# Performance work log

Hardware: AMD Instinct MI355X
Metric: run time of the kernel (lower is better)

## Reference

```python
import jax, jax.numpy as jnp
import numpy as np

N = 50000      # nodes
E = 800000     # edges
G = 256        # graphs in batch
D_IN = 128     # input_dim
H = 128        # node_hidden_dim
FC = 128       # fc_hidden_dim
OUT = 2        # out_dim
EPS = 1e-5


def _lin_init(key, fan_in, fan_out, bias=True):
    kw, kb = jax.random.split(key)
    w = jax.random.normal(kw, (fan_in, fan_out), jnp.float32) / np.sqrt(fan_in)
    if bias:
        b = jax.random.normal(kb, (fan_out,), jnp.float32) * 0.01
        return w, b
    return w


def setup_inputs() -> dict:
    key = jax.random.key(0)
    ks = jax.random.split(key, 16)
    x = jax.random.normal(ks[0], (N, D_IN), jnp.float32)
    edge_index = jax.random.randint(ks[1], (2, E), 0, N, jnp.int32)
    batch = jnp.sort(jax.random.randint(ks[2], (N,), 0, G, jnp.int32))
    edge_attr = jax.random.uniform(ks[3], (E, 1), jnp.float32)
    # GraphConv params: lin_rel (with bias) + lin_root (no bias)
    w_rel1, b_rel1 = _lin_init(ks[4], D_IN, H)
    w_root1 = _lin_init(ks[5], D_IN, H, bias=False)
    w_rel2, b_rel2 = _lin_init(ks[6], H, 2 * H)
    w_root2 = _lin_init(ks[7], H, 2 * H, bias=False)
    w_rel3, b_rel3 = _lin_init(ks[8], 2 * H, 3 * H)
    w_root3 = _lin_init(ks[9], 2 * H, 3 * H, bias=False)
    # BatchNorm affine params
    gamma1 = jnp.ones((H,), jnp.float32);      beta1 = jnp.zeros((H,), jnp.float32)
    gamma2 = jnp.ones((2 * H,), jnp.float32);  beta2 = jnp.zeros((2 * H,), jnp.float32)
    gamma3 = jnp.ones((3 * H,), jnp.float32);  beta3 = jnp.zeros((3 * H,), jnp.float32)
    # FC head: lin1 in = 3H+6H+9H = 18H
    w_lin1, b_lin1 = _lin_init(ks[10], 18 * H, FC)
    w_lin2, b_lin2 = _lin_init(ks[11], FC, OUT)
    w_lin3, b_lin3 = _lin_init(ks[12], OUT, OUT)
    return dict(x=x, edge_index=edge_index, batch=batch, edge_attr=edge_attr,
                w_rel1=w_rel1, b_rel1=b_rel1, w_root1=w_root1,
                w_rel2=w_rel2, b_rel2=b_rel2, w_root2=w_root2,
                w_rel3=w_rel3, b_rel3=b_rel3, w_root3=w_root3,
                gamma1=gamma1, beta1=beta1, gamma2=gamma2, beta2=beta2,
                gamma3=gamma3, beta3=beta3,
                w_lin1=w_lin1, b_lin1=b_lin1, w_lin2=w_lin2, b_lin2=b_lin2,
                w_lin3=w_lin3, b_lin3=b_lin3)


def _bn(h, gamma, beta):
    # training-mode BatchNorm1d over node axis
    mu = h.mean(0)
    var = h.var(0)
    return (h - mu) * jax.lax.rsqrt(var + EPS) * gamma + beta


def _gconv(h, src, dst, ew, w_rel, b_rel, w_root):
    # PyG GraphConv: lin_rel(sum_j ew_ij * x_j) + lin_root(x_i)
    agg = jax.ops.segment_sum(h[src] * ew[:, None], dst, num_segments=N)
    return agg @ w_rel + b_rel + h @ w_root


def _pool3(h, batch):
    # concat of global max / mean / add pooling per graph
    s = jax.ops.segment_sum(h, batch, num_segments=G)
    cnt = jax.ops.segment_sum(jnp.ones((h.shape[0], 1), h.dtype), batch, num_segments=G)
    mean = s / jnp.maximum(cnt, 1.0)
    m = jax.ops.segment_max(h, batch, num_segments=G)
    m = jnp.where(cnt > 0, m, 0.0)  # guard empty segments
    return jnp.concatenate([m, mean, s], axis=1)


def reference(x, edge_index, batch, edge_attr,
              w_rel1, b_rel1, w_root1, w_rel2, b_rel2, w_root2,
              w_rel3, b_rel3, w_root3,
              gamma1, beta1, gamma2, beta2, gamma3, beta3,
              w_lin1, b_lin1, w_lin2, b_lin2, w_lin3, b_lin3):
    ew = jnp.transpose(edge_attr, (1, 0))[0]            # [E]
    src, dst = edge_index[0], edge_index[1]
    h = _bn(jax.nn.leaky_relu(_gconv(x, src, dst, ew, w_rel1, b_rel1, w_root1)), gamma1, beta1)
    x1 = _pool3(h, batch)
    h = _bn(jax.nn.leaky_relu(_gconv(h, src, dst, ew, w_rel2, b_rel2, w_root2)), gamma2, beta2)
    x2 = _pool3(h, batch)
    h = _bn(jax.nn.leaky_relu(_gconv(h, src, dst, ew, w_rel3, b_rel3, w_root3)), gamma3, beta3)
    x3 = _pool3(h, batch)
    z = jnp.concatenate([x1, x2, x3], axis=1)           # [G, 18H]
    z = jax.nn.relu(z @ w_lin1 + b_lin1)                # dropout is identity in eval
    z = jax.nn.relu(z @ w_lin2 + b_lin2)
    return jax.nn.log_softmax(z @ w_lin3 + b_lin3, axis=-1)
```

## Files before the change

kernel.cpp:

```cpp
#include <hip/hip_runtime.h>
#include <cstdint>
#include <cstddef>

#define N_NODES 50000
#define M_PAD   50048
#define MB_TILES 391
#define N_EDGES 800000
#define N_GRAPH 256
#define Z_DIM   2304
#define NREP    16
#define POOL_TOT (N_GRAPH * (128 + 256 + 384))
#define PP_L1 (MB_TILES * 1 * 2 * 2 * 128)
#define PP_L2 (MB_TILES * 2 * 2 * 2 * 128)
#define PP_L3 (MB_TILES * 3 * 2 * 2 * 128)
#define PP_TOT (PP_L1 + PP_L2 + PP_L3)

static constexpr float LEAKY  = 0.01f;
static constexpr float BN_EPS = 1e-5f;
static constexpr float FNEG   = -3.4e38f;
static constexpr float FPOS   =  3.4e38f;

typedef short short8 __attribute__((ext_vector_type(8)));
typedef float floatx4 __attribute__((ext_vector_type(4)));
typedef const __attribute__((address_space(1))) unsigned int* gas_ptr;
typedef __attribute__((address_space(3))) unsigned int* las_ptr;
typedef unsigned long long ull;

__device__ __forceinline__ unsigned short f2b(float f) {
  union { float f; unsigned int u; } v; v.f = f;
  unsigned int u = v.u;
  unsigned int r = (u + 0x7FFFu + ((u >> 16) & 1u)) >> 16;
  return (unsigned short)r;
}
__device__ __forceinline__ float b2f(unsigned short h) {
  union { unsigned int u; float f; } v; v.u = ((unsigned int)h) << 16;
  return v.f;
}
__device__ __forceinline__ unsigned fkey(float x) {
  unsigned k = __float_as_uint(x);
  return k ^ ((k & 0x80000000u) ? 0xFFFFFFFFu : 0x80000000u);
}
__device__ __forceinline__ float kdec(unsigned k) {
  k ^= (k & 0x80000000u) ? 0x80000000u : 0xFFFFFFFFu;
  return __uint_as_float(k);
}


__global__ void init_all_kernel(int* __restrict__ cntR, int* __restrict__ gcnt,
                                float* __restrict__ sums_all,
                                unsigned* __restrict__ pmaxk, unsigned* __restrict__ pmink,
                                float* __restrict__ psumg) {
  const int i = blockIdx.x * blockDim.x + threadIdx.x;
  if (i < NREP * N_NODES) cntR[i] = 0;
  if (i < N_GRAPH) gcnt[i] = 0;
  if (i < 2 * (128 + 256 + 384)) sums_all[i] = 0.f;
  if (i < POOL_TOT) { pmaxk[i] = 0u; pmink[i] = 0xFFFFFFFFu; psumg[i] = 0.f; }
}


__global__ void hist_rep_kernel(const int* __restrict__ idx, int* __restrict__ cntR, int n) {
  int i = blockIdx.x * blockDim.x + threadIdx.x;
  if (i < n) {
    const int rep = blockIdx.x & (NREP - 1);
    atomicAdd(&cntR[rep * N_NODES + idx[i]], 1);
  }
}

__global__ __launch_bounds__(256) void scan1_fused_kernel(int* __restrict__ cntR,
                                                          int* __restrict__ out,
                                                          int* __restrict__ part, int n) {
  __shared__ int sm[256];
  const int t = threadIdx.x;
  const int base = blockIdx.x * 1024 + t * 4;
  int v[4] = {0, 0, 0, 0};
#pragma unroll
  for (int j = 0; j < 4; ++j) {
    const int d = base + j;
    if (d < n) {
      int s = 0;
#pragma unroll
      for (int r = 0; r < NREP; ++r) {
        const int c = cntR[r * N_NODES + d];
        cntR[r * N_NODES + d] = s;
        s += c;
      }
      v[j] = s;
    }
  }
  const int tsum = v[0] + v[1] + v[2] + v[3];
  sm[t] = tsum;
  __syncthreads();
  for (int off = 1; off < 256; off <<= 1) {
    int x = (t >= off) ? sm[t - off] : 0;
    __syncthreads();
    sm[t] += x;
    __syncthreads();
  }
  const int excl = sm[t] - tsum;
  if (base     < n) out[base]     = excl;
  if (base + 1 < n) out[base + 1] = excl + v[0];
  if (base + 2 < n) out[base + 2] = excl + v[0] + v[1];
  if (base + 3 < n) out[base + 3] = excl + v[0] + v[1] + v[2];
  if (t == 255) part[blockIdx.x] = sm[255];
}

__global__ __launch_bounds__(256) void scan2_kernel(int* __restrict__ part, int nb,
                                                    int* __restrict__ total_out) {
  __shared__ int sm[256];
  const int t = threadIdx.x;
  const int v = (t < nb) ? part[t] : 0;
  sm[t] = v;
  __syncthreads();
  for (int off = 1; off < 256; off <<= 1) {
    int x = (t >= off) ? sm[t - off] : 0;
    __syncthreads();
    sm[t] += x;
    __syncthreads();
  }
  if (t < nb) part[t] = sm[t] - v;
  if (t == 255) *total_out = sm[255];
}

__global__ void scan3_cursor_kernel(int* __restrict__ out, const int* __restrict__ part,
                                    int* __restrict__ cntR, int n) {
  int i = blockIdx.x * blockDim.x + threadIdx.x;
  if (i >= n) return;
  const int rp = out[i] + part[i >> 10];
  out[i] = rp;
#pragma unroll
  for (int r = 0; r < NREP; ++r) cntR[r * N_NODES + i] += rp;
}

__global__ void bucket_kernel(const int* __restrict__ src, const int* __restrict__ dst,
                              const float* __restrict__ ew, int* __restrict__ cntR,
                              ull* __restrict__ epack, int E) {
  int e = blockIdx.x * blockDim.x + threadIdx.x;
  if (e < E) {
    const int rep = blockIdx.x & (NREP - 1);
    const int d = dst[e];
    const int p = atomicAdd(&cntR[rep * N_NODES + d], 1);
    epack[p] = ((ull)__float_as_uint(ew[e]) << 32) | (unsigned)src[e];
  }
}

__global__ __launch_bounds__(256) void hist_batch_kernel(const int* __restrict__ idx,
                                                         int* __restrict__ cnt, int n) {
  __shared__ int lh[N_GRAPH];
  lh[threadIdx.x] = 0;
  __syncthreads();
  int i = blockIdx.x * blockDim.x + threadIdx.x;
  if (i < n) atomicAdd(&lh[idx[i]], 1);
  __syncthreads();
  const int v = lh[threadIdx.x];
  if (v) atomicAdd(&cnt[threadIdx.x], v);
}

__global__ __launch_bounds__(256) void scan256_kernel(const int* __restrict__ cnt,
                                                      int* __restrict__ gptr) {
  __shared__ int sm[256];
  const int t = threadIdx.x;
  const int v = cnt[t];
  sm[t] = v;
  __syncthreads();
  for (int off = 1; off < 256; off <<= 1) {
    int x = (t >= off) ? sm[t - off] : 0;
    __syncthreads();
    sm[t] += x;
    __syncthreads();
  }
  gptr[t] = sm[t] - v;
  if (t == 255) gptr[256] = sm[255];
}


__global__ __launch_bounds__(256) void prep1_kernel(
    const float* __restrict__ x, unsigned short* __restrict__ xb, int npair,
    const float* __restrict__ wrel, const float* __restrict__ wroot,
    const float* __restrict__ brel,
    unsigned short* __restrict__ wt, float* __restrict__ u, float* __restrict__ v) {
  if (blockIdx.x >= 128) {
    const int i = (blockIdx.x - 128) * 256 + threadIdx.x;
    if (i < npair) {
      float2 vv = *(const float2*)(x + 2 * (size_t)i);
      ((unsigned int*)xb)[i] = (unsigned int)f2b(vv.x) | ((unsigned int)f2b(vv.y) << 16);
    }
    return;
  }
  __shared__ float redu[256];
  __shared__ float redv[256];
  const int n = blockIdx.x;
  const int K = 128, N = 128, K2 = 256;
  float us = 0.f, vs = 0.f;
  for (int k = threadIdx.x; k < K2; k += 256) {
    const int kk = (k < K) ? k : k - K;
    const float w = (k < K) ? wrel[(size_t)kk * N + n] : wroot[(size_t)kk * N + n];
    wt[(size_t)n * K2 + k] = f2b(w);
    (void)kk;
  }
  redu[threadIdx.x] = us; redv[threadIdx.x] = vs;
  __syncthreads();
  for (int o = 128; o > 0; o >>= 1) {
    if (threadIdx.x < o) {
      redu[threadIdx.x] += redu[threadIdx.x + o];
      redv[threadIdx.x] += redv[threadIdx.x + o];
    }
    __syncthreads();
  }
  if (threadIdx.x == 0) { u[n] = redu[0]; v[n] = brel[n] + redv[0]; }
}

__global__ __launch_bounds__(256) void wt_build_kernel(
    const float* __restrict__ wrel, const float* __restrict__ wroot,
    const float* __restrict__ brel, const float* __restrict__ sums_prev,
    const float* __restrict__ gamma_prev, const float* __restrict__ beta_prev,
    unsigned short* __restrict__ wt, float* __restrict__ u, float* __restrict__ v,
    int K, int N) {
  __shared__ float redu[256];
  __shared__ float redv[256];
  const int n = blockIdx.x;
  const int K2 = 2 * K;
  const float inv_n = 1.f / (float)N_NODES;
  float us = 0.f, vs = 0.f;
  for (int k = threadIdx.x; k < K2; k += 256) {
    const int kk = (k < K) ? k : k - K;
    const float w = (k < K) ? wrel[(size_t)kk * N + n] : wroot[(size_t)kk * N + n];
    float sc = 1.f, sh = 0.f;
    if (sums_prev) {
      const float mu  = sums_prev[kk] * inv_n;
      const float var = sums_prev[K + kk] * inv_n - mu * mu;
      sc = rsqrtf(var + BN_EPS) * gamma_prev[kk];
      sh = beta_prev[kk] - mu * sc;
    }
    wt[(size_t)n * K2 + k] = f2b(w * sc);
    if (k < K) us += sh * w; else vs += sh * w;
  }
  redu[threadIdx.x] = us; redv[threadIdx.x] = vs;
  __syncthreads();
  for (int o = 128; o > 0; o >>= 1) {
    if (threadIdx.x < o) {
      redu[threadIdx.x] += redu[threadIdx.x + o];
      redv[threadIdx.x] += redv[threadIdx.x + o];
    }
    __syncthreads();
  }
  if (threadIdx.x == 0) { u[n] = redu[0]; v[n] = brel[n] + redv[0]; }
}


template <int D>
__global__ void agg_bf16_kernel(const unsigned short* __restrict__ h,
                                const int* __restrict__ rowptr,
                                const ull* __restrict__ epack,
                                unsigned short* __restrict__ agg,
                                float* __restrict__ degw_out) {
  int gid  = blockIdx.x * blockDim.x + threadIdx.x;
  int node = gid >> 6;
  int lane = threadIdx.x & 63;
  if (node >= N_NODES) return;
  const int beg = rowptr[node], end = rowptr[node + 1];
  constexpr int NP = D / 128;
  float acc0[NP], acc1[NP];
#pragma unroll
  for (int i = 0; i < NP; ++i) { acc0[i] = 0.f; acc1[i] = 0.f; }
  float wsum = 0.f;

  for (int c0 = beg; c0 < end; c0 += 64) {
    const int cn = min(64, end - c0);
    ull pk = 0;
    if (lane < cn) pk = epack[c0 + lane];
    const int   su = (int)(unsigned)pk;
    const float wf = __uint_as_float((unsigned)(pk >> 32));
    const int ng = (cn + 7) >> 3;
    for (int g = 0; g < ng; ++g) {
      int ss[8]; float wv[8];
#pragma unroll
      for (int j = 0; j < 8; ++j) {
        ss[j] = __shfl(su, g * 8 + j);
        wv[j] = __shfl(wf, g * 8 + j);
      }
      unsigned uu[8][NP];
#pragma unroll
      for (int j = 0; j < 8; ++j) {
        const unsigned int* row = (const unsigned int*)(h + (size_t)ss[j] * D);
#pragma unroll
        for (int i = 0; i < NP; ++i) uu[j][i] = row[lane + 64 * i];
      }
#pragma unroll
      for (int j = 0; j < 8; ++j) {
        wsum += wv[j];
#pragma unroll
        for (int i = 0; i < NP; ++i) {
          acc0[i] += b2f((unsigned short)(uu[j][i] & 0xFFFF)) * wv[j];
          acc1[i] += b2f((unsigned short)(uu[j][i] >> 16)) * wv[j];
        }
      }
    }
  }

  unsigned int* o = (unsigned int*)(agg + (size_t)node * D);
#pragma unroll
  for (int i = 0; i < NP; ++i)
    o[lane + 64 * i] = (unsigned int)f2b(acc0[i]) | ((unsigned int)f2b(acc1[i]) << 16);
  if (degw_out != nullptr && lane == 0) degw_out[node] = wsum;
}


__global__ __launch_bounds__(256) void gemm_mfma_kernel(
    const unsigned short* __restrict__ Aagg, const unsigned short* __restrict__ Ah,
    const unsigned short* __restrict__ Wt,
    const float* __restrict__ u, const float* __restrict__ v,
    const float* __restrict__ degw, const int* __restrict__ batch,
    unsigned short* __restrict__ outH, float* __restrict__ sums,
    unsigned* __restrict__ pmaxk, unsigned* __restrict__ pmink,
    float* __restrict__ psumg,
    float* __restrict__ ppmax, float* __restrict__ ppmin, float* __restrict__ ppsum,
    int M, int K, int N) {
  __shared__ char smem[40960];
  unsigned short* AsBase = (unsigned short*)smem;
  unsigned short* BsBase = (unsigned short*)(smem + 24576);
  float* col_s = (float*)smem;
  float* dws   = (float*)(smem + 1024);
  int*   gbs   = (int*)(smem + 1536);

  const int NT = N >> 7;
  const int id = blockIdx.x;
  const int xcd = id & 7;
  const int q   = id >> 3;
  const int m_tile = (q / NT) * 8 + xcd;
  if (m_tile >= MB_TILES) return;
  const int m0 = m_tile * 128;
  const int nt2 = q % NT;
  const int n0 = nt2 * 128;

  const int t  = threadIdx.x;
  const int lane = t & 63;
  const int w    = t >> 6;
  const int wm   = (w & 1) * 64;
  const int wn   = (w >> 1) * 64;
  const int l16  = lane & 15;
  const int lq   = lane >> 4;
  const int K2   = 2 * K;

  const int lrow  = lane >> 2;
  const int lslot = lane & 3;

  floatx4 acc[4][4];
#pragma unroll
  for (int i = 0; i < 4; ++i)
#pragma unroll
    for (int j = 0; j < 4; ++j) acc[i][j] = (floatx4){0.f, 0.f, 0.f, 0.f};

  auto stage_A = [&](unsigned short* Ab, int k0) {
    const unsigned short* Asrc;
    int kbase;
    if (k0 < K) { Asrc = Aagg; kbase = k0; } else { Asrc = Ah; kbase = k0 - K; }
#pragma unroll
    for (int qq = 0; qq < 2; ++qq) {
      const int row = w * 32 + qq * 16 + lrow;
      const int gc  = (lslot ^ ((row >> 1) & 3)) * 8;
      const unsigned short* gA = Asrc + (size_t)(m0 + row) * K + kbase + gc;
      __builtin_amdgcn_global_load_lds((gas_ptr)gA, (las_ptr)(Ab + (w * 32 + qq * 16) * 32),
                                       16, 0, 0);
    }
  };
  auto stage_B = [&](unsigned short* Bb, int k0) {
#pragma unroll
    for (int qq = 0; qq < 2; ++qq) {
      const int row = w * 32 + qq * 16 + lrow;
      const int gc  = (lslot ^ ((row >> 1) & 3)) * 8;
      const unsigned short* gB = Wt + (size_t)(n0 + row) * K2 + k0 + gc;
      __builtin_amdgcn_global_load_lds((gas_ptr)gB, (las_ptr)(Bb + (w * 32 + qq * 16) * 32),
                                       16, 0, 0);
    }
  };

  auto compute = [&](const unsigned short* Ab, const unsigned short* Bb) {
    short8 af[4], bfr[4];
#pragma unroll
    for (int i = 0; i < 4; ++i) {
      const int r = wm + i * 16 + l16;
      af[i] = *(const short8*)(Ab + r * 32 + (lq ^ ((r >> 1) & 3)) * 8);
    }
#pragma unroll
    for (int j = 0; j < 4; ++j) {
      const int r = wn + j * 16 + l16;
      bfr[j] = *(const short8*)(Bb + r * 32 + (lq ^ ((r >> 1) & 3)) * 8);
    }
    __builtin_amdgcn_s_setprio(1);
#pragma unroll
    for (int i = 0; i < 4; ++i)
#pragma unroll
      for (int j = 0; j < 4; ++j)
        acc[i][j] = __builtin_amdgcn_mfma_f32_16x16x32_bf16(af[i], bfr[j], acc[i][j], 0, 0, 0);
    __builtin_amdgcn_s_setprio(0);
  };

  const int NSTEP = K2 >> 5;

  unsigned short *A0 = AsBase, *A1 = AsBase + 4096, *A2 = AsBase + 8192;
  unsigned short *B0 = BsBase, *B1 = BsBase + 4096;

  stage_A(A0, 0);
  stage_B(B0, 0);
  stage_A(A1, 1 << 5);

  for (int s = 0; s < NSTEP - 1; ++s) {
    asm volatile("s_waitcnt vmcnt(2)" ::: "memory");
    __builtin_amdgcn_s_barrier();
    __builtin_amdgcn_sched_barrier(0);
    stage_B(B1, (s + 1) << 5);
    if (s + 2 < NSTEP) stage_A(A2, (s + 2) << 5);
    compute(A0, B0);
    unsigned short* tA = A0; A0 = A1; A1 = A2; A2 = tA;
    unsigned short* tB = B0; B0 = B1; B1 = tB;
  }
  asm volatile("s_waitcnt vmcnt(0)" ::: "memory");
  __builtin_amdgcn_s_barrier();
  __builtin_amdgcn_sched_barrier(0);
  compute(A0, B0);

  __syncthreads();
  col_s[t] = 0.f;
  if (t < 128) {
    const int m = m0 + t;
    dws[t] = (m < M) ? degw[m] : 0.f;
    gbs[t] = (m < M) ? batch[m] : -1;
  }
  __syncthreads();

  float uu[4], vv[4];
#pragma unroll
  for (int j = 0; j < 4; ++j) {
    const int n = n0 + wn + j * 16 + l16;
    uu[j] = u[n]; vv[j] = v[n];
  }

  const bool wout = (outH != nullptr);
  const int lastr = min(127, M - 1 - m0);
  const int gmin = gbs[0];
  const int gmax = gbs[lastr];

  float ts[4]  = {0.f, 0.f, 0.f, 0.f};
  float tss[4] = {0.f, 0.f, 0.f, 0.f};
  float px0[4], pn0[4], ps0[4], px1[4], pn1[4], ps1[4];
#pragma unroll
  for (int j = 0; j < 4; ++j) {
    px0[j] = FNEG; pn0[j] = FPOS; ps0[j] = 0.f;
    px1[j] = FNEG; pn1[j] = FPOS; ps1[j] = 0.f;
  }

#pragma unroll
  for (int i = 0; i < 4; ++i) {
    const int lrow2 = wm + i * 16 + lq * 4;
#pragma unroll
    for (int r = 0; r < 4; ++r) {
      const int row = lrow2 + r;
      const bool live = (m0 + row < M);
      const int gv = gbs[row];
      const float dwr = dws[row];
      const bool in0 = live && (gv == gmin);
      const bool in1 = live && (gmax != gmin) && (gv == gmax);
#pragma unroll
      for (int j = 0; j < 4; ++j) {
        const int n = n0 + wn + j * 16 + l16;
        float val = acc[i][j][r] + vv[j] + dwr * uu[j];
        val = val > 0.f ? val : LEAKY * val;
        acc[i][j][r] = val;
        if (live) {
          if (wout) outH[(size_t)(m0 + row) * N + n] = f2b(val);
          ts[j]  += val;
          tss[j] += val * val;
        }
        if (in0) { px0[j] = fmaxf(px0[j], val); pn0[j] = fminf(pn0[j], val); ps0[j] += val; }
        if (in1) { px1[j] = fmaxf(px1[j], val); pn1[j] = fminf(pn1[j], val); ps1[j] += val; }
      }
    }
  }

  const int half = w & 1;
#pragma unroll
  for (int j = 0; j < 4; ++j) {
    float a = ts[j], b = tss[j];
    a += __shfl_xor(a, 16); a += __shfl_xor(a, 32);
    b += __shfl_xor(b, 16); b += __shfl_xor(b, 32);
    float x0 = px0[j], n0v = pn0[j], s0v = ps0[j];
    x0 = fmaxf(x0, __shfl_xor(x0, 16)); x0 = fmaxf(x0, __shfl_xor(x0, 32));
    n0v = fminf(n0v, __shfl_xor(n0v, 16)); n0v = fminf(n0v, __shfl_xor(n0v, 32));
    s0v += __shfl_xor(s0v, 16); s0v += __shfl_xor(s0v, 32);
    float x1 = px1[j], n1v = pn1[j], s1v = ps1[j];
    x1 = fmaxf(x1, __shfl_xor(x1, 16)); x1 = fmaxf(x1, __shfl_xor(x1, 32));
    n1v = fminf(n1v, __shfl_xor(n1v, 16)); n1v = fminf(n1v, __shfl_xor(n1v, 32));
    s1v += __shfl_xor(s1v, 16); s1v += __shfl_xor(s1v, 32);
    if (lq == 0) {
      const int ci = wn + j * 16 + l16;
      atomicAdd(&col_s[ci], a);
      atomicAdd(&col_s[128 + ci], b);
      const size_t tb = (size_t)(m_tile * NT + nt2) * 2;
      const size_t sb0 = ((tb + 0) * 2 + half) * 128 + ci;
      const size_t sb1 = ((tb + 1) * 2 + half) * 128 + ci;
      ppmax[sb0] = x0;  ppmin[sb0] = n0v; ppsum[sb0] = s0v;
      ppmax[sb1] = x1;  ppmin[sb1] = n1v; ppsum[sb1] = s1v;
    }
  }

  if (gmax > gmin + 1) {
    for (int g = gmin + 1; g < gmax; ++g) {
#pragma unroll
      for (int j = 0; j < 4; ++j) {
        float mx = FNEG, mn = FPOS, sm = 0.f;
#pragma unroll
        for (int i = 0; i < 4; ++i) {
          const int lrow2 = wm + i * 16 + lq * 4;
#pragma unroll
          for (int r = 0; r < 4; ++r) {
            const int row = lrow2 + r;
            if (m0 + row < M && gbs[row] == g) {
              const float val = acc[i][j][r];
              mx = fmaxf(mx, val); mn = fminf(mn, val); sm += val;
            }
          }
        }
        mx = fmaxf(mx, __shfl_xor(mx, 16)); mx = fmaxf(mx, __shfl_xor(mx, 32));
        mn = fminf(mn, __shfl_xor(mn, 16)); mn = fminf(mn, __shfl_xor(mn, 32));
        sm += __shfl_xor(sm, 16); sm += __shfl_xor(sm, 32);
        if (lq == 0 && mx > -3.3e38f) {
          const size_t pi = (size_t)g * N + (n0 + wn + j * 16 + l16);
          atomicMax(&pmaxk[pi], fkey(mx));
          atomicMin(&pmink[pi], fkey(mn));
          atomicAdd(&psumg[pi], sm);
        }
      }
    }
  }

  __syncthreads();
  if (t < 128) {
    atomicAdd(&sums[n0 + t], col_s[t]);
    atomicAdd(&sums[N + n0 + t], col_s[128 + t]);
  }
}


__global__ __launch_bounds__(1024) void finalize_fc_kernel(
    const unsigned* __restrict__ pmaxk, const unsigned* __restrict__ pmink,
    const float* __restrict__ psumg,
    const float* __restrict__ ppmax, const float* __restrict__ ppmin,
    const float* __restrict__ ppsum,
    const float* __restrict__ sums_all,
    const float* __restrict__ gamma1, const float* __restrict__ beta1,
    const float* __restrict__ gamma2, const float* __restrict__ beta2,
    const float* __restrict__ gamma3, const float* __restrict__ beta3,
    const int* __restrict__ gptr, const int* __restrict__ batch,
    const float* __restrict__ w1, const float* __restrict__ b1,
    const float* __restrict__ w2, const float* __restrict__ b2,
    const float* __restrict__ w3, const float* __restrict__ b3,
    float* __restrict__ out) {
  __shared__ float zs[Z_DIM];
  __shared__ float part[8][128];
  __shared__ float h1s[128];
  __shared__ float red[128][2];
  __shared__ float y2[2];
  const int g = blockIdx.x;
  const int t = threadIdx.x;
  const int cnt = gptr[g + 1] - gptr[g];

  if (t < 768) {
    int C, zoff, c, PO, NTL;
    size_t ppo;
    const float *sums, *gamma, *beta;
    if (t < 128) {
      C = 128; zoff = 0; c = t; PO = 0; NTL = 1; ppo = 0;
      sums = sums_all; gamma = gamma1; beta = beta1;
    } else if (t < 384) {
      C = 256; zoff = 384; c = t - 128; PO = N_GRAPH * 128; NTL = 2; ppo = PP_L1;
      sums = sums_all + 2 * 128; gamma = gamma2; beta = beta2;
    } else {
      C = 384; zoff = 1152; c = t - 384; PO = N_GRAPH * (128 + 256); NTL = 3;
      ppo = PP_L1 + PP_L2;
      sums = sums_all + 2 * (128 + 256); gamma = gamma3; beta = beta3;
    }
    const int i = PO + g * C + c;

    float mx = FNEG, mn = FPOS, sm = psumg[i];
    {
      const unsigned pk = pmaxk[i];
      if (pk != 0u) mx = kdec(pk);
      const unsigned nk = pmink[i];
      if (nk != 0xFFFFFFFFu) mn = kdec(nk);
    }
    if (cnt > 0) {
      const int mt_lo = gptr[g] >> 7;
      const int mt_hi = (gptr[g + 1] - 1) >> 7;
      const int nt = c >> 7, cc = c & 127;
      for (int mt = mt_lo; mt <= mt_hi; ++mt) {
        const int g0 = batch[mt << 7];
        int grel = (g == g0) ? 0 : -1;
        if (grel < 0) {
          const int lastm = min((mt << 7) + 127, N_NODES - 1);
          if (g == batch[lastm]) grel = 1;
        }
        if (grel >= 0) {
          const size_t b0 = ppo + (((size_t)(mt * NTL + nt) * 2 + grel) * 2 + 0) * 128 + cc;
          const size_t b1v = b0 + 128;
          mx = fmaxf(mx, fmaxf(ppmax[b0], ppmax[b1v]));
          mn = fminf(mn, fminf(ppmin[b0], ppmin[b1v]));
          sm += ppsum[b0] + ppsum[b1v];
        }
      }
    }

    const float inv_n = 1.f / (float)N_NODES;
    const float mu  = sums[c] * inv_n;
    const float var = sums[C + c] * inv_n - mu * mu;
    const float sc  = rsqrtf(var + BN_EPS) * gamma[c];
    const float sh  = beta[c] - mu * sc;
    const float zmax = (sc >= 0.f ? mx : mn) * sc + sh;
    const float zsum = sm * sc + (float)cnt * sh;
    zs[zoff + c]         = (cnt > 0) ? zmax : 0.f;
    zs[zoff + C + c]     = zsum / (float)(cnt > 0 ? cnt : 1);
    zs[zoff + 2 * C + c] = zsum;
  }
  __syncthreads();

  const int c  = t & 127;
  const int ks = t >> 7;
  constexpr int KCH = Z_DIM / 8;
  const int k0 = ks * KCH;
  float acc = 0.f;
#pragma unroll 4
  for (int k = k0; k < k0 + KCH; ++k) acc += zs[k] * w1[(size_t)k * 128 + c];
  part[ks][c] = acc;
  __syncthreads();

  if (t < 128) {
    float s = b1[t];
#pragma unroll
    for (int i = 0; i < 8; ++i) s += part[i][t];
    h1s[t] = fmaxf(s, 0.f);
  }
  __syncthreads();
  if (t < 128) {
    red[t][0] = h1s[t] * w2[t * 2 + 0];
    red[t][1] = h1s[t] * w2[t * 2 + 1];
  }
  __syncthreads();
  if (t < 2) {
    float s = b2[t];
    for (int k = 0; k < 128; ++k) s += red[k][t];
    y2[t] = fmaxf(s, 0.f);
  }
  __syncthreads();
  if (t == 0) {
    const float z0 = y2[0] * w3[0] + y2[1] * w3[2] + b3[0];
    const float z1 = y2[0] * w3[1] + y2[1] * w3[3] + b3[1];
    const float m  = fmaxf(z0, z1);
    const float lse = m + logf(expf(z0 - m) + expf(z1 - m));
    out[g * 2 + 0] = z0 - lse;
    out[g * 2 + 1] = z1 - lse;
  }
}


extern "C" void kernel_launch(void* const* d_in, const int* in_sizes, int n_in,
                              void* d_out, int out_size, void* d_ws, size_t ws_size,
                              hipStream_t stream) {
  (void)in_sizes; (void)n_in; (void)out_size; (void)ws_size;
  const float* x        = (const float*)d_in[0];
  const int*   eidx     = (const int*)d_in[1];
  const int*   batch    = (const int*)d_in[2];
  const float* eattr    = (const float*)d_in[3];
  const float* w_rel1   = (const float*)d_in[4];
  const float* b_rel1   = (const float*)d_in[5];
  const float* w_root1  = (const float*)d_in[6];
  const float* w_rel2   = (const float*)d_in[7];
  const float* b_rel2   = (const float*)d_in[8];
  const float* w_root2  = (const float*)d_in[9];
  const float* w_rel3   = (const float*)d_in[10];
  const float* b_rel3   = (const float*)d_in[11];
  const float* w_root3  = (const float*)d_in[12];
  const float* gamma1   = (const float*)d_in[13];
  const float* beta1    = (const float*)d_in[14];
  const float* gamma2   = (const float*)d_in[15];
  const float* beta2    = (const float*)d_in[16];
  const float* gamma3   = (const float*)d_in[17];
  const float* beta3    = (const float*)d_in[18];
  const float* w_lin1   = (const float*)d_in[19];
  const float* b_lin1   = (const float*)d_in[20];
  const float* w_lin2   = (const float*)d_in[21];
  const float* b_lin2   = (const float*)d_in[22];
  const float* w_lin3   = (const float*)d_in[23];
  const float* b_lin3   = (const float*)d_in[24];

  const int* src = eidx;
  const int* dst = eidx + N_EDGES;
  float* outp = (float*)d_out;

  char* ws = (char*)d_ws;
  size_t off = 0;
  auto alloc = [&](size_t bytes) -> void* {
    void* p = ws + off;
    off += (bytes + 255) & ~(size_t)255;
    return p;
  };
  int*   rowptr = (int*)alloc((N_NODES + 1) * sizeof(int));
  int*   cntR   = (int*)alloc((size_t)NREP * N_NODES * sizeof(int));
  int*   gptr   = (int*)alloc((N_GRAPH + 1) * sizeof(int));
  int*   gcnt   = (int*)alloc(N_GRAPH * sizeof(int));
  int*   part   = (int*)alloc(256 * sizeof(int));
  ull*   epack  = (ull*)alloc((size_t)N_EDGES * sizeof(ull));
  float* degw   = (float*)alloc(N_NODES * sizeof(float));
  float* sums_all = (float*)alloc(2 * (128 + 256 + 384) * sizeof(float));
  unsigned* pmaxk = (unsigned*)alloc((size_t)POOL_TOT * 4);
  unsigned* pmink = (unsigned*)alloc((size_t)POOL_TOT * 4);
  float*    psumg = (float*)alloc((size_t)POOL_TOT * 4);
  float* ppmax = (float*)alloc((size_t)PP_TOT * 4);
  float* ppmin = (float*)alloc((size_t)PP_TOT * 4);
  float* ppsum = (float*)alloc((size_t)PP_TOT * 4);
  unsigned short* xb   = (unsigned short*)alloc((size_t)M_PAD * 128 * 2);
  unsigned short* hp1  = (unsigned short*)alloc((size_t)M_PAD * 128 * 2);
  unsigned short* hp2  = (unsigned short*)alloc((size_t)M_PAD * 256 * 2);
  unsigned short* aggb = (unsigned short*)alloc((size_t)M_PAD * 256 * 2);
  unsigned short* wt1 = (unsigned short*)alloc((size_t)128 * 256 * 2);
  unsigned short* wt2 = (unsigned short*)alloc((size_t)256 * 256 * 2);
  unsigned short* wt3 = (unsigned short*)alloc((size_t)384 * 512 * 2);
  float* u1 = (float*)alloc(128 * sizeof(float));
  float* v1 = (float*)alloc(128 * sizeof(float));
  float* u2 = (float*)alloc(256 * sizeof(float));
  float* v2 = (float*)alloc(256 * sizeof(float));
  float* u3 = (float*)alloc(384 * sizeof(float));
  float* v3 = (float*)alloc(384 * sizeof(float));

  float* sums1 = sums_all;
  float* sums2 = sums_all + 2 * 128;
  float* sums3 = sums_all + 2 * (128 + 256);
  const int PO1 = 0, PO2 = N_GRAPH * 128, PO3 = N_GRAPH * (128 + 256);

  const int EB = (N_EDGES + 255) / 256;
  const int NB = (N_NODES + 255) / 256;
  const int SB = (N_NODES + 1023) / 1024;

  init_all_kernel<<<(NREP * N_NODES + 255) / 256, 256, 0, stream>>>(
      cntR, gcnt, sums_all, pmaxk, pmink, psumg);

  hist_rep_kernel<<<EB, 256, 0, stream>>>(dst, cntR, N_EDGES);
  scan1_fused_kernel<<<SB, 256, 0, stream>>>(cntR, rowptr, part, N_NODES);
  scan2_kernel<<<1, 256, 0, stream>>>(part, SB, rowptr + N_NODES);
  scan3_cursor_kernel<<<NB, 256, 0, stream>>>(rowptr, part, cntR, N_NODES);
  bucket_kernel<<<EB, 256, 0, stream>>>(src, dst, eattr, cntR, epack, N_EDGES);

  hist_batch_kernel<<<NB, 256, 0, stream>>>(batch, gcnt, N_NODES);
  scan256_kernel<<<1, 256, 0, stream>>>(gcnt, gptr);

  const int npair = N_NODES * 128 / 2;
  prep1_kernel<<<128 + (npair + 255) / 256, 256, 0, stream>>>(
      x, xb, npair, w_rel1, w_root1, b_rel1, wt1, u1, v1);

  const int aggBlocks = (N_NODES * 64 + 255) / 256;

  agg_bf16_kernel<128><<<aggBlocks, 256, 0, stream>>>(xb, rowptr, epack, aggb, degw);
  gemm_mfma_kernel<<<392 * 1, 256, 0, stream>>>(aggb, xb, wt1, u1, v1, degw, batch,
                                                hp1, sums1, pmaxk + PO1, pmink + PO1,
                                                psumg + PO1, ppmax, ppmin, ppsum,
                                                N_NODES, 128, 128);
  wt_build_kernel<<<256, 256, 0, stream>>>(w_rel2, w_root2, b_rel2, sums1, gamma1, beta1,
                                           wt2, u2, v2, 128, 256);

  agg_bf16_kernel<128><<<aggBlocks, 256, 0, stream>>>(hp1, rowptr, epack, aggb, nullptr);
  gemm_mfma_kernel<<<392 * 2, 256, 0, stream>>>(aggb, hp1, wt2, u2, v2, degw, batch,
                                                hp2, sums2, pmaxk + PO2, pmink + PO2,
                                                psumg + PO2, ppmax + PP_L1, ppmin + PP_L1,
                                                ppsum + PP_L1, N_NODES, 128, 256);
  wt_build_kernel<<<384, 256, 0, stream>>>(w_rel3, w_root3, b_rel3, sums2, gamma2, beta2,
                                           wt3, u3, v3, 256, 384);

  agg_bf16_kernel<256><<<aggBlocks, 256, 0, stream>>>(hp2, rowptr, epack, aggb, nullptr);
  gemm_mfma_kernel<<<392 * 3, 256, 0, stream>>>(aggb, hp2, wt3, u3, v3, degw, batch,
                                                (unsigned short*)nullptr, sums3,
                                                pmaxk + PO3, pmink + PO3, psumg + PO3,
                                                ppmax + PP_L1 + PP_L2, ppmin + PP_L1 + PP_L2,
                                                ppsum + PP_L1 + PP_L2, N_NODES, 256, 384);

  finalize_fc_kernel<<<N_GRAPH, 1024, 0, stream>>>(
      pmaxk, pmink, psumg, ppmax, ppmin, ppsum, sums_all,
      gamma1, beta1, gamma2, beta2, gamma3, beta3, gptr, batch,
      w_lin1, b_lin1, w_lin2, b_lin2, w_lin3, b_lin3, outp);
}
```

Before: 483.7 us.

## Cut launches: fuse scan2 into scan3, merge weight build with aggregation, drop batch histogram

Removes several small kernels. scan2 is folded into scan3_cursor, where each block sums the block partials it needs from shared memory, and the total edge count is written as a constant. The per-layer weight-build kernel is merged into the aggregation kernel as extra leading blocks. The batch histogram and scan256 are replaced by per-graph binary searches on the sorted batch array inside finalize. The intent is to cut launch and serialization overhead from tiny kernels, at the cost of redundant partial-sum loops and the assumption that batch is sorted.

```diff
diff --git a/kernel.cpp b/kernel.cpp
--- a/kernel.cpp
+++ b/kernel.cpp
@@ -44,15 +44,19 @@
   k ^= (k & 0x80000000u) ? 0x80000000u : 0xFFFFFFFFu;
   return __uint_as_float(k);
 }
-
-
-__global__ void init_all_kernel(int* __restrict__ cntR, int* __restrict__ gcnt,
+__device__ __forceinline__ int lbound(const int* __restrict__ b, int n, int val) {
+  int lo = 0, hi = n;
+  while (lo < hi) { const int mid = (lo + hi) >> 1; if (b[mid] < val) lo = mid + 1; else hi = mid; }
+  return lo;
+}
+
+
+__global__ void init_all_kernel(int* __restrict__ cntR,
                                 float* __restrict__ sums_all,
                                 unsigned* __restrict__ pmaxk, unsigned* __restrict__ pmink,
                                 float* __restrict__ psumg) {
   const int i = blockIdx.x * blockDim.x + threadIdx.x;
   if (i < NREP * N_NODES) cntR[i] = 0;
-  if (i < N_GRAPH) gcnt[i] = 0;
   if (i < 2 * (128 + 256 + 384)) sums_all[i] = 0.f;
   if (i < POOL_TOT) { pmaxk[i] = 0u; pmink[i] = 0xFFFFFFFFu; psumg[i] = 0.f; }
 }
@@ -104,28 +108,21 @@
   if (t == 255) part[blockIdx.x] = sm[255];
 }
 
-__global__ __launch_bounds__(256) void scan2_kernel(int* __restrict__ part, int nb,
-                                                    int* __restrict__ total_out) {
-  __shared__ int sm[256];
+__global__ __launch_bounds__(256) void scan3_cursor_kernel(int* __restrict__ out,
+                                                           const int* __restrict__ part,
+                                                           int* __restrict__ cntR,
+                                                           int n, int nb) {
+  __shared__ int ps[64];
   const int t = threadIdx.x;
-  const int v = (t < nb) ? part[t] : 0;
-  sm[t] = v;
-  __syncthreads();
-  for (int off = 1; off < 256; off <<= 1) {
-    int x = (t >= off) ? sm[t - off] : 0;
-    __syncthreads();
-    sm[t] += x;
-    __syncthreads();
-  }
-  if (t < nb) part[t] = sm[t] - v;
-  if (t == 255) *total_out = sm[255];
-}
-
-__global__ void scan3_cursor_kernel(int* __restrict__ out, const int* __restrict__ part,
-                                    int* __restrict__ cntR, int n) {
-  int i = blockIdx.x * blockDim.x + threadIdx.x;
+  if (t < nb) ps[t] = part[t];
+  __syncthreads();
+  const int pb = blockIdx.x >> 2;
+  int myp = 0;
+  for (int k = 0; k < pb; ++k) myp += ps[k];
+  const int i = blockIdx.x * 256 + t;
+  if (i == 0) out[n] = N_EDGES;
   if (i >= n) return;
-  const int rp = out[i] + part[i >> 10];
+  const int rp = out[i] + myp;
   out[i] = rp;
 #pragma unroll
   for (int r = 0; r < NREP; ++r) cntR[r * N_NODES + i] += rp;
@@ -141,35 +138,6 @@
     const int p = atomicAdd(&cntR[rep * N_NODES + d], 1);
     epack[p] = ((ull)__float_as_uint(ew[e]) << 32) | (unsigned)src[e];
   }
-}
-
-__global__ __launch_bounds__(256) void hist_batch_kernel(const int* __restrict__ idx,
-                                                         int* __restrict__ cnt, int n) {
-  __shared__ int lh[N_GRAPH];
-  lh[threadIdx.x] = 0;
-  __syncthreads();
-  int i = blockIdx.x * blockDim.x + threadIdx.x;
-  if (i < n) atomicAdd(&lh[idx[i]], 1);
-  __syncthreads();
-  const int v = lh[threadIdx.x];
-  if (v) atomicAdd(&cnt[threadIdx.x], v);
-}
-
-__global__ __launch_bounds__(256) void scan256_kernel(const int* __restrict__ cnt,
-                                                      int* __restrict__ gptr) {
-  __shared__ int sm[256];
-  const int t = threadIdx.x;
-  const int v = cnt[t];
-  sm[t] = v;
-  __syncthreads();
-  for (int off = 1; off < 256; off <<= 1) {
-    int x = (t >= off) ? sm[t - off] : 0;
-    __syncthreads();
-    sm[t] += x;
-    __syncthreads();
-  }
-  gptr[t] = sm[t] - v;
-  if (t == 255) gptr[256] = sm[255];
 }
 
 
@@ -186,66 +154,107 @@
     }
     return;
   }
-  __shared__ float redu[256];
-  __shared__ float redv[256];
   const int n = blockIdx.x;
   const int K = 128, N = 128, K2 = 256;
-  float us = 0.f, vs = 0.f;
   for (int k = threadIdx.x; k < K2; k += 256) {
     const int kk = (k < K) ? k : k - K;
     const float w = (k < K) ? wrel[(size_t)kk * N + n] : wroot[(size_t)kk * N + n];
     wt[(size_t)n * K2 + k] = f2b(w);
-    (void)kk;
-  }
-  redu[threadIdx.x] = us; redv[threadIdx.x] = vs;
-  __syncthreads();
-  for (int o = 128; o > 0; o >>= 1) {
-    if (threadIdx.x < o) {
-      redu[threadIdx.x] += redu[threadIdx.x + o];
-      redv[threadIdx.x] += redv[threadIdx.x + o];
-    }
-    __syncthreads();
-  }
-  if (threadIdx.x == 0) { u[n] = redu[0]; v[n] = brel[n] + redv[0]; }
-}
-
-__global__ __launch_bounds__(256) void wt_build_kernel(
+  }
+  if (threadIdx.x == 0) { u[n] = 0.f; v[n] = brel[n]; }
+}
+
+
+template <int D>
+__global__ __launch_bounds__(256) void wtagg_kernel(
     const float* __restrict__ wrel, const float* __restrict__ wroot,
     const float* __restrict__ brel, const float* __restrict__ sums_prev,
     const float* __restrict__ gamma_prev, const float* __restrict__ beta_prev,
     unsigned short* __restrict__ wt, float* __restrict__ u, float* __restrict__ v,
-    int K, int N) {
-  __shared__ float redu[256];
-  __shared__ float redv[256];
-  const int n = blockIdx.x;
-  const int K2 = 2 * K;
-  const float inv_n = 1.f / (float)N_NODES;
-  float us = 0.f, vs = 0.f;
-  for (int k = threadIdx.x; k < K2; k += 256) {
-    const int kk = (k < K) ? k : k - K;
-    const float w = (k < K) ? wrel[(size_t)kk * N + n] : wroot[(size_t)kk * N + n];
-    float sc = 1.f, sh = 0.f;
-    if (sums_prev) {
+    int K, int N, int NW,
+    const unsigned short* __restrict__ h, const int* __restrict__ rowptr,
+    const ull* __restrict__ epack, unsigned short* __restrict__ agg,
+    float* __restrict__ degw_out) {
+  if ((int)blockIdx.x < NW) {
+    __shared__ float redu[256];
+    __shared__ float redv[256];
+    const int n = blockIdx.x;
+    const int K2 = 2 * K;
+    const float inv_n = 1.f / (float)N_NODES;
+    float us = 0.f, vs = 0.f;
+    for (int k = threadIdx.x; k < K2; k += 256) {
+      const int kk = (k < K) ? k : k - K;
+      const float w = (k < K) ? wrel[(size_t)kk * N + n] : wroot[(size_t)kk * N + n];
       const float mu  = sums_prev[kk] * inv_n;
       const float var = sums_prev[K + kk] * inv_n - mu * mu;
-      sc = rsqrtf(var + BN_EPS) * gamma_prev[kk];
-      sh = beta_prev[kk] - mu * sc;
-    }
-    wt[(size_t)n * K2 + k] = f2b(w * sc);
-    if (k < K) us += sh * w; else vs += sh * w;
-  }
-  redu[threadIdx.x] = us; redv[threadIdx.x] = vs;
-  __syncthreads();
-  for (int o = 128; o > 0; o >>= 1) {
-    if (threadIdx.x < o) {
-      redu[threadIdx.x] += redu[threadIdx.x + o];
-      redv[threadIdx.x] += redv[threadIdx.x + o];
-    }
+      const float sc  = rsqrtf(var + BN_EPS) * gamma_prev[kk];
+      const float sh  = beta_prev[kk] - mu * sc;
+      wt[(size_t)n * K2 + k] = f2b(w * sc);
+      if (k < K) us += sh * w; else vs += sh * w;
+    }
+    redu[threadIdx.x] = us; redv[threadIdx.x] = vs;
     __syncthreads();
-  }
-  if (threadIdx.x == 0) { u[n] = redu[0]; v[n] = brel[n] + redv[0]; }
-}
-
+    for (int o = 128; o > 0; o >>= 1) {
+      if (threadIdx.x < o) {
+        redu[threadIdx.x] += redu[threadIdx.x + o];
+        redv[threadIdx.x] += redv[threadIdx.x + o];
+      }
+      __syncthreads();
+    }
+    if (threadIdx.x == 0) { u[n] = redu[0]; v[n] = brel[n] + redv[0]; }
+    return;
+  }
+
+  int gid  = (blockIdx.x - NW) * 256 + threadIdx.x;
+  int node = gid >> 6;
+  int lane = threadIdx.x & 63;
+  if (node >= N_NODES) return;
+  const int beg = rowptr[node], end = rowptr[node + 1];
+  constexpr int NP = D / 128;
+  float acc0[NP], acc1[NP];
+#pragma unroll
+  for (int i = 0; i < NP; ++i) { acc0[i] = 0.f; acc1[i] = 0.f; }
+  float wsum = 0.f;
+
+  for (int c0 = beg; c0 < end; c0 += 64) {
+    const int cn = min(64, end - c0);
+    ull pk = 0;
+    if (lane < cn) pk = epack[c0 + lane];
+    const int   su = (int)(unsigned)pk;
+    const float wf = __uint_as_float((unsigned)(pk >> 32));
+    const int ng = (cn + 7) >> 3;
+    for (int g = 0; g < ng; ++g) {
+      int ss[8]; float wv[8];
+#pragma unroll
+      for (int j = 0; j < 8; ++j) {
+        ss[j] = __shfl(su, g * 8 + j);
+        wv[j] = __shfl(wf, g * 8 + j);
+      }
+      unsigned uu[8][NP];
+#pragma unroll
+      for (int j = 0; j < 8; ++j) {
+        const unsigned int* row = (const unsigned int*)(h + (size_t)ss[j] * D);
+#pragma unroll
+        for (int i = 0; i < NP; ++i) uu[j][i] = row[lane + 64 * i];
+      }
+#pragma unroll
+      for (int j = 0; j < 8; ++j) {
+        wsum += wv[j];
+#pragma unroll
+        for (int i = 0; i < NP; ++i) {
+          acc0[i] += b2f((unsigned short)(uu[j][i] & 0xFFFF)) * wv[j];
+          acc1[i] += b2f((unsigned short)(uu[j][i] >> 16)) * wv[j];
+        }
+      }
+    }
+  }
+
+  unsigned int* o = (unsigned int*)(agg + (size_t)node * D);
+#pragma unroll
+  for (int i = 0; i < NP; ++i)
+    o[lane + 64 * i] = (unsigned int)f2b(acc0[i]) | ((unsigned int)f2b(acc1[i]) << 16);
+  if (degw_out != nullptr && lane == 0) degw_out[node] = wsum;
+}
 
 template <int D>
 __global__ void agg_bf16_kernel(const unsigned short* __restrict__ h,
@@ -550,7 +559,7 @@
     const float* __restrict__ gamma1, const float* __restrict__ beta1,
     const float* __restrict__ gamma2, const float* __restrict__ beta2,
     const float* __restrict__ gamma3, const float* __restrict__ beta3,
-    const int* __restrict__ gptr, const int* __restrict__ batch,
+    const int* __restrict__ batch,
     const float* __restrict__ w1, const float* __restrict__ b1,
     const float* __restrict__ w2, const float* __restrict__ b2,
     const float* __restrict__ w3, const float* __restrict__ b3,
@@ -560,9 +569,14 @@
   __shared__ float h1s[128];
   __shared__ float red[128][2];
   __shared__ float y2[2];
+  __shared__ int gb2[2];
   const int g = blockIdx.x;
   const int t = threadIdx.x;
-  const int cnt = gptr[g + 1] - gptr[g];
+
+  if (t < 2) gb2[t] = lbound(batch, N_NODES, g + t);
+  __syncthreads();
+  const int glo = gb2[0], ghi = gb2[1];
+  const int cnt = ghi - glo;
 
   if (t < 768) {
     int C, zoff, c, PO, NTL;
@@ -589,8 +603,8 @@
       if (nk != 0xFFFFFFFFu) mn = kdec(nk);
     }
     if (cnt > 0) {
-      const int mt_lo = gptr[g] >> 7;
-      const int mt_hi = (gptr[g + 1] - 1) >> 7;
+      const int mt_lo = glo >> 7;
+      const int mt_hi = (ghi - 1) >> 7;
       const int nt = c >> 7, cc = c & 127;
       for (int mt = mt_lo; mt <= mt_hi; ++mt) {
         const int g0 = batch[mt << 7];
@@ -704,8 +718,6 @@
   };
   int*   rowptr = (int*)alloc((N_NODES + 1) * sizeof(int));
   int*   cntR   = (int*)alloc((size_t)NREP * N_NODES * sizeof(int));
-  int*   gptr   = (int*)alloc((N_GRAPH + 1) * sizeof(int));
-  int*   gcnt   = (int*)alloc(N_GRAPH * sizeof(int));
   int*   part   = (int*)alloc(256 * sizeof(int));
   ull*   epack  = (ull*)alloc((size_t)N_EDGES * sizeof(ull));
   float* degw   = (float*)alloc(N_NODES * sizeof(float));
@@ -740,16 +752,12 @@
   const int SB = (N_NODES + 1023) / 1024;
 
   init_all_kernel<<<(NREP * N_NODES + 255) / 256, 256, 0, stream>>>(
-      cntR, gcnt, sums_all, pmaxk, pmink, psumg);
+      cntR, sums_all, pmaxk, pmink, psumg);
 
   hist_rep_kernel<<<EB, 256, 0, stream>>>(dst, cntR, N_EDGES);
   scan1_fused_kernel<<<SB, 256, 0, stream>>>(cntR, rowptr, part, N_NODES);
-  scan2_kernel<<<1, 256, 0, stream>>>(part, SB, rowptr + N_NODES);
-  scan3_cursor_kernel<<<NB, 256, 0, stream>>>(rowptr, part, cntR, N_NODES);
+  scan3_cursor_kernel<<<NB, 256, 0, stream>>>(rowptr, part, cntR, N_NODES, SB);
   bucket_kernel<<<EB, 256, 0, stream>>>(src, dst, eattr, cntR, epack, N_EDGES);
-
-  hist_batch_kernel<<<NB, 256, 0, stream>>>(batch, gcnt, N_NODES);
-  scan256_kernel<<<1, 256, 0, stream>>>(gcnt, gptr);
 
   const int npair = N_NODES * 128 / 2;
   prep1_kernel<<<128 + (npair + 255) / 256, 256, 0, stream>>>(
@@ -762,18 +770,18 @@
                                                 hp1, sums1, pmaxk + PO1, pmink + PO1,
                                                 psumg + PO1, ppmax, ppmin, ppsum,
                                                 N_NODES, 128, 128);
-  wt_build_kernel<<<256, 256, 0, stream>>>(w_rel2, w_root2, b_rel2, sums1, gamma1, beta1,
-                                           wt2, u2, v2, 128, 256);
-
-  agg_bf16_kernel<128><<<aggBlocks, 256, 0, stream>>>(hp1, rowptr, epack, aggb, nullptr);
+
+  wtagg_kernel<128><<<256 + aggBlocks, 256, 0, stream>>>(
+      w_rel2, w_root2, b_rel2, sums1, gamma1, beta1, wt2, u2, v2, 128, 256, 256,
+      hp1, rowptr, epack, aggb, nullptr);
   gemm_mfma_kernel<<<392 * 2, 256, 0, stream>>>(aggb, hp1, wt2, u2, v2, degw, batch,
                                                 hp2, sums2, pmaxk + PO2, pmink + PO2,
                                                 psumg + PO2, ppmax + PP_L1, ppmin + PP_L1,
                                                 ppsum + PP_L1, N_NODES, 128, 256);
-  wt_build_kernel<<<384, 256, 0, stream>>>(w_rel3, w_root3, b_rel3, sums2, gamma2, beta2,
-                                           wt3, u3, v3, 256, 384);
-
-  agg_bf16_kernel<256><<<aggBlocks, 256, 0, stream>>>(hp2, rowptr, epack, aggb, nullptr);
+
+  wtagg_kernel<256><<<384 + aggBlocks, 256, 0, stream>>>(
+      w_rel3, w_root3, b_rel3, sums2, gamma2, beta2, wt3, u3, v3, 256, 384, 384,
+      hp2, rowptr, epack, aggb, nullptr);
   gemm_mfma_kernel<<<392 * 3, 256, 0, stream>>>(aggb, hp2, wt3, u3, v3, degw, batch,
                                                 (unsigned short*)nullptr, sums3,
                                                 pmaxk + PO3, pmink + PO3, psumg + PO3,
@@ -782,6 +790,6 @@
 
   finalize_fc_kernel<<<N_GRAPH, 1024, 0, stream>>>(
       pmaxk, pmink, psumg, ppmax, ppmin, ppsum, sums_all,
-      gamma1, beta1, gamma2, beta2, gamma3, beta3, gptr, batch,
+      gamma1, beta1, gamma2, beta2, gamma3, beta3, batch,
       w_lin1, b_lin1, w_lin2, b_lin2, w_lin3, b_lin3, outp);
 }
```

Result: faster. 467.6 us (-3.3%).
